# Optimization experiments

Measured on AMD Instinct MI355X. Metric: run time of the kernel, lower is better.

## Reference

```python
import jax, jax.numpy as jnp
import numpy as np

B, C, H, W = 64, 1024, 14, 14
DK, DV, NH = 512, 512, 8
NCLS = 32  # each class appears B//NCLS = 2 times -> no singleton labels


def setup_inputs() -> dict:
    key = jax.random.key(0)
    k1, k2, k3, k4 = jax.random.split(key, 4)
    dkh = DK // NH
    x = jax.random.normal(k1, (B, C, H, W), jnp.float32)
    W_qkv = jax.random.normal(k2, (2 * DK + DV, C), jnp.float32) * 0.02
    b_qkv = jnp.zeros((2 * DK + DV,), jnp.float32)
    key_rel_w = jax.random.normal(k3, (2 * W - 1, dkh), jnp.float32)
    key_rel_h = jax.random.normal(k4, (2 * H - 1, dkh), jnp.float32)
    # label-based pair index (training path of the torch module)
    rng = np.random.default_rng(0)
    labels = np.repeat(np.arange(NCLS), B // NCLS)
    rng.shuffle(labels)
    pair = np.empty(B, np.int32)
    for j in range(B):
        idx = np.nonzero(labels == labels[j])[0]
        pos = int(np.nonzero(idx == j)[0][0])
        pair[j] = idx[(pos + 1) % len(idx)]
    return {"x": x, "W_qkv": W_qkv, "b_qkv": b_qkv,
            "key_rel_w": key_rel_w, "key_rel_h": key_rel_h,
            "pair_index": jnp.asarray(pair)}


def rel_to_abs(x):
    b, nh, L, _ = x.shape
    x = jnp.pad(x, ((0, 0), (0, 0), (0, 0), (0, 1)))            # [b,nh,L,2L]
    flat = x.reshape(b, nh, L * 2 * L)
    flat = jnp.pad(flat, ((0, 0), (0, 0), (0, L - 1)))
    return flat.reshape(b, nh, L + 1, 2 * L - 1)[:, :, :L, L - 1:]


def relative_logits_1d(q, rel_k, Hd, Wd, nh, case):
    # q: [b, nh, Hd, Wd, dkh]; rel_k: [2*Wd-1, dkh]
    b = q.shape[0]
    rel = jnp.einsum('bhxyd,md->bhxym', q, rel_k)                 # [b,nh,Hd,Wd,2Wd-1]
    rel = rel_to_abs(rel.reshape(b, nh * Hd, Wd, 2 * Wd - 1))     # [b,nh*Hd,Wd,Wd]
    rel = rel.reshape(b, nh, Hd, Wd, Wd)[:, :, :, None]           # [b,nh,Hd,1,Wd,Wd]
    rel = jnp.broadcast_to(rel, (b, nh, Hd, Hd, Wd, Wd))
    if case == 'w':
        rel = jnp.swapaxes(rel, 3, 4)
    else:  # 'h'
        rel = jnp.swapaxes(rel, 2, 4)
        rel = jnp.swapaxes(rel, 4, 5)
        rel = jnp.swapaxes(rel, 3, 5)
    return rel.reshape(b, nh, Hd * Wd, Hd * Wd)


def reference(x, W_qkv, b_qkv, key_rel_w, key_rel_h, pair_index):
    b, c, h, w = x.shape
    nh, dk, dv = NH, DK, DV
    dkh = dk // nh
    # 1x1 conv == channel GEMM
    qkv = jnp.einsum('bchw,oc->bohw', x, W_qkv) + b_qkv[None, :, None, None]
    q = qkv[:, :dk].reshape(b, nh, dkh, h, w) * dkh ** (-0.5)
    k = qkv[:, dk:2 * dk].reshape(b, nh, dkh, h, w)
    flat_q = q.reshape(b, nh, dkh, h * w)
    flat_k = k.reshape(b, nh, dkh, h * w)
    flat_q = flat_q / jnp.linalg.norm(flat_q, axis=2, keepdims=True)
    flat_k = flat_k / jnp.linalg.norm(flat_k, axis=2, keepdims=True)
    q_avg = (flat_q[pair_index] + flat_q) * 0.5
    logits = jnp.einsum('bndq,bndk->bnqk', q_avg, flat_k)         # [b,nh,HW,HW]
    q_perm = jnp.transpose(q, (0, 1, 3, 4, 2))                    # [b,nh,h,w,dkh]
    w_rel = relative_logits_1d(q_perm, key_rel_w, h, w, nh, 'w')
    h_rel = relative_logits_1d(jnp.swapaxes(q_perm, 2, 3), key_rel_h, w, h, nh, 'h')
    logits = logits + h_rel + w_rel
    # combine_heads + mean over dim 1 == mean over (nh, query) axes
    mean_logits = jnp.mean(logits.reshape(b, nh, h * w, h, w), axis=(1, 2))  # [b,h,w]
    attn = jax.nn.softmax(mean_logits.reshape(b, -1), axis=-1).reshape(b, 1, h, w)
    return jnp.concatenate((x / 49.0, x * attn), axis=1)
```

## Files before the change

### kernel.cpp

```cpp
#include <hip/hip_runtime.h>
#include <hip/hip_bf16.h>
#include <math.h>

typedef unsigned short ushort_t;
using bf16x8 = __attribute__((ext_vector_type(8))) short;
using f32x4  = __attribute__((ext_vector_type(4))) float;

#define BATCH 64
#define CIN   1024
#define HH    14
#define WW    14
#define P     196
#define NHEAD 8
#define DKH   64
#define PPAD  224

#define OFF_Y16  0
#define N_Y16_F  6422528
#define OFF_XB   (OFF_Y16 + N_Y16_F)
#define N_XB_F   7340032
#define OFF_WB   (OFF_XB + N_XB_F)
#define N_WB_F   524288
#define OFF_INK  (OFF_WB + N_WB_F)
#define N_INK    (BATCH*NHEAD*P)
#define OFF_SQ   (OFF_INK + N_INK)
#define N_SQ     (BATCH*NHEAD*DKH)
#define OFF_QH   (OFF_SQ + N_SQ)
#define N_QH     (BATCH*HH*DKH)
#define OFF_QW   (OFF_QH + N_QH)
#define N_QW     (BATCH*WW*DKH)
#define OFF_AW   (OFF_QW + N_QW)
#define N_AW     (BATCH*WW)
#define OFF_AH   (OFF_AW + N_AW)
#define N_AH     (BATCH*HH)
#define OFF_ML   (OFF_AH + N_AH)
#define N_ML     (BATCH*P)
#define OFF_ATTN (OFF_ML + N_ML)
#define N_ATTN   (BATCH*P)
#define ZERO_FLOATS 129024

__device__ __forceinline__ ushort_t f2bf(float f) {
    union { float f; unsigned u; } v; v.f = f;
    unsigned r = v.u + 0x7fffu + ((v.u >> 16) & 1u);
    return (ushort_t)(r >> 16);
}
__device__ __forceinline__ float bf2f(ushort_t u) {
    union { unsigned u; float f; } v; v.u = ((unsigned)u) << 16; return v.f;
}
__device__ __forceinline__ void gll16(const ushort_t* g, ushort_t* l) {
    __builtin_amdgcn_global_load_lds(
        (const __attribute__((address_space(1))) void*)g,
        (__attribute__((address_space(3))) void*)l, 16, 0, 0);
}

__global__ __launch_bounds__(256) void k_convW(const float* __restrict__ Wq,
                                               ushort_t* __restrict__ Wb) {
    int i = blockIdx.x * 256 + threadIdx.x;
    const float4 v = ((const float4*)Wq)[i];
    ushort4 o;
    o.x = f2bf(v.x); o.y = f2bf(v.y); o.z = f2bf(v.z); o.w = f2bf(v.w);
    ((ushort4*)Wb)[i] = o;
}

__global__ __launch_bounds__(256) void k_trans(const float* __restrict__ x,
                                               ushort_t* __restrict__ Xb) {
    const int c0 = blockIdx.x * 64, p0 = blockIdx.y * 32, b = blockIdx.z;
    const int t = threadIdx.x;
    __shared__ float tile[64][33];
    const float* xb = x + (size_t)b * (CIN * P);
#pragma unroll
    for (int it = 0; it < 8; ++it) {
        int idx = t + it * 256;
        int c_l = idx >> 5, p_l = idx & 31;
        int p = p0 + p_l;
        tile[c_l][p_l] = (p < P) ? xb[(size_t)(c0 + c_l) * P + p] : 0.f;
    }
    __syncthreads();
    int c_chunk = (t & 7) * 8, p_l = t >> 3;
    ushort_t buf[8];
#pragma unroll
    for (int e = 0; e < 8; ++e) buf[e] = f2bf(tile[c_chunk + e][p_l]);
    *(uint4*)(Xb + ((size_t)b * PPAD + p0 + p_l) * CIN + c0 + c_chunk) = *(uint4*)buf;
}

__global__ __launch_bounds__(256, 4) void k_mfma(const ushort_t* __restrict__ Xb,
                                                 const ushort_t* __restrict__ Wb,
                                                 const float* __restrict__ bias,
                                                 ushort_t* __restrict__ Y16) {
    const int o0 = blockIdx.x * 128, r0 = blockIdx.y * 128;
    const int tid = threadIdx.x, w = tid >> 6, l = tid & 63;
    const int wm = w >> 1, wn = w & 1;
    __shared__ ushort_t xa[128 * 64];
    __shared__ ushort_t xw[128 * 64];
    f32x4 acc[4][4];
#pragma unroll
    for (int mf = 0; mf < 4; ++mf)
#pragma unroll
        for (int j = 0; j < 4; ++j) acc[mf][j] = (f32x4){0.f, 0.f, 0.f, 0.f};

    const ushort_t* Ab = Xb + (size_t)r0 * CIN;
    const ushort_t* Bb = Wb + (size_t)o0 * CIN;
    const int lrow = l >> 3, lch = (l & 7) * 8;

    for (int c0 = 0; c0 < CIN; c0 += 64) {
        if (c0) __syncthreads();
#pragma unroll
        for (int i = 0; i < 4; ++i) {
            int rowblk = (w * 4 + i) * 8;
            gll16(Ab + (size_t)(rowblk + lrow) * CIN + c0 + lch, xa + rowblk * 64);
        }
#pragma unroll
        for (int i = 0; i < 4; ++i) {
            int rowblk = (w * 4 + i) * 8;
            gll16(Bb + (size_t)(rowblk + lrow) * CIN + c0 + lch, xw + rowblk * 64);
        }
        __syncthreads();
#pragma unroll
        for (int kk = 0; kk < 2; ++kk) {
            bf16x8 bfrag[4];
#pragma unroll
            for (int j = 0; j < 4; ++j)
                bfrag[j] = *(const bf16x8*)(xw + (wn * 64 + j * 16 + (l & 15)) * 64 + kk * 32 + (l >> 4) * 8);
#pragma unroll
            for (int mf = 0; mf < 4; ++mf) {
                bf16x8 afrag = *(const bf16x8*)(xa + (wm * 64 + mf * 16 + (l & 15)) * 64 + kk * 32 + (l >> 4) * 8);
#pragma unroll
                for (int j = 0; j < 4; ++j)
                    acc[mf][j] = __builtin_amdgcn_mfma_f32_16x16x32_bf16(afrag, bfrag[j], acc[mf][j], 0, 0, 0);
            }
        }
    }
    const int oc = l & 15, pq = (l >> 4) * 4;
#pragma unroll
    for (int j = 0; j < 4; ++j) {
        int o = o0 + wn * 64 + j * 16 + oc;
        float bo = bias[o];
#pragma unroll
        for (int mf = 0; mf < 4; ++mf) {
            int r = r0 + wm * 64 + mf * 16 + pq;
            int b = r / PPAD;
            int p = r - b * PPAD;
            if (p < P) {
                ushort_t tmp[4];
#pragma unroll
                for (int e = 0; e < 4; ++e) tmp[e] = f2bf(acc[mf][j][e] + bo);
                *(ushort4*)(Y16 + ((size_t)b * 1024 + o) * P + p) = *(ushort4*)tmp;
            }
        }
    }
}

__global__ __launch_bounds__(256) void k_norm(const ushort_t* __restrict__ Y16,
                                              float* __restrict__ ink_g,
                                              float* __restrict__ sq_g,
                                              float* __restrict__ qh_g,
                                              float* __restrict__ qw_g) {
    const int bn = blockIdx.x, b = bn >> 3, n = bn & 7;
    const int tid = threadIdx.x;
    __shared__ ushort_t qs[64 * P];
    __shared__ float inq_s[P];
    __shared__ float part[4][64];
    const uint* Yq = (const uint*)(Y16 + ((size_t)b * 1024 + n * 64) * P);
    for (int i = tid; i < 64 * (P / 2); i += 256) ((uint*)qs)[i] = Yq[i];
    const ushort_t* Yk = Y16 + ((size_t)b * 1024 + 512 + n * 64) * P;
    const int p = tid, pc = (p < P) ? p : 0;
    float sk = 0.f;
    for (int d = 0; d < 64; ++d) { float v = bf2f(Yk[d * P + pc]); sk = fmaf(v, v, sk); }
    __syncthreads();
    float sq = 0.f;
    for (int d = 0; d < 64; ++d) { float v = bf2f(qs[d * P + pc]); sq = fmaf(v, v, sq); }
    if (p < P) { ink_g[bn * P + p] = rsqrtf(sk); inq_s[p] = rsqrtf(sq); }
    __syncthreads();
    {
        int d = tid & 63, q4 = tid >> 6;
        float s = 0.f;
        for (int i = 0; i < 49; ++i) {
            int pp = q4 * 49 + i;
            s = fmaf(bf2f(qs[d * P + pp]), inq_s[pp], s);
        }
        part[q4][d] = s;
    }
    __syncthreads();
    if (tid < 64) sq_g[bn * 64 + tid] = part[0][tid] + part[1][tid] + part[2][tid] + part[3][tid];
    for (int it = tid; it < 896; it += 256) {
        int d = it & 63, xx = it >> 6;
        float s = 0.f;
#pragma unroll
        for (int y = 0; y < WW; ++y) s += bf2f(qs[d * P + xx * WW + y]);
        atomicAdd(&qh_g[(b * HH + xx) * 64 + d], s * 0.125f);
    }
    for (int it = tid; it < 896; it += 256) {
        int d = it & 63, y = it >> 6;
        float s = 0.f;
#pragma unroll
        for (int xx = 0; xx < HH; ++xx) s += bf2f(qs[d * P + xx * WW + y]);
        atomicAdd(&qw_g[(b * WW + y) * 64 + d], s * 0.125f);
    }
}

__global__ __launch_bounds__(512) void k_rel(const float* __restrict__ qh_g,
                                             const float* __restrict__ qw_g,
                                             const float* __restrict__ relw,
                                             const float* __restrict__ relh,
                                             float* __restrict__ Aw_g,
                                             float* __restrict__ Ah_g) {
    const int b = blockIdx.x, t = threadIdx.x;
    if (t < 196) {
        int X = t / 14, y = t % 14;
        const float* qw = qw_g + (b * WW + y) * 64;
        const float* rw = relw + (13 + X - y) * 64;
        float s = 0.f;
#pragma unroll 8
        for (int d = 0; d < 64; ++d) s = fmaf(qw[d], rw[d], s);
        atomicAdd(&Aw_g[b * WW + X], s);
    } else if (t >= 256 && t < 452) {
        int i = t - 256, X = i / 14, xr = i % 14;
        const float* qh = qh_g + (b * HH + xr) * 64;
        const float* rh = relh + (13 + X - xr) * 64;
        float s = 0.f;
#pragma unroll 8
        for (int d = 0; d < 64; ++d) s = fmaf(qh[d], rh[d], s);
        atomicAdd(&Ah_g[b * HH + X], s);
    }
}

__global__ __launch_bounds__(256) void k_dot(const ushort_t* __restrict__ Y16,
                                             const float* __restrict__ ink_g,
                                             const float* __restrict__ sq_g,
                                             const int*   __restrict__ pair,
                                             float* __restrict__ ml) {
    const int bn = blockIdx.x, b = bn >> 3, n = bn & 7;
    const int tid = threadIdx.x;
    __shared__ float Sav[64];
    if (tid < 64) {
        int pb = pair[b];
        Sav[tid] = 0.5f * (sq_g[bn * 64 + tid] + sq_g[(pb * 8 + n) * 64 + tid]);
    }
    __syncthreads();
    const int p = tid;
    if (p < P) {
        const ushort_t* Yk = Y16 + ((size_t)b * 1024 + 512 + n * 64) * P;
        float s = 0.f;
#pragma unroll 8
        for (int d = 0; d < 64; ++d) s = fmaf(Sav[d], bf2f(Yk[d * P + p]), s);
        atomicAdd(&ml[b * P + p], s * ink_g[bn * P + p]);
    }
}

__global__ __launch_bounds__(256) void k_soft(const float* __restrict__ ml,
                                              const float* __restrict__ Aw_g,
                                              const float* __restrict__ Ah_g,
                                              float* __restrict__ attn_g) {
    const int b = blockIdx.x, tid = threadIdx.x;
    __shared__ float red[256];
    const int p = tid;
    float v = -1e30f;
    if (p < P) v = (ml[b * P + p] + Ah_g[b * HH + p / WW] + Aw_g[b * WW + p % WW]) * (1.f / 1568.f);
    red[tid] = v; __syncthreads();
    for (int s = 128; s > 0; s >>= 1) { if (tid < s) red[tid] = fmaxf(red[tid], red[tid + s]); __syncthreads(); }
    float mx = red[0]; __syncthreads();
    float e = (p < P) ? expf(v - mx) : 0.f;
    red[tid] = e; __syncthreads();
    for (int s = 128; s > 0; s >>= 1) { if (tid < s) red[tid] += red[tid + s]; __syncthreads(); }
    if (p < P) attn_g[b * P + p] = e / red[0];
}

__global__ __launch_bounds__(256) void k_out(const float* __restrict__ x,
                                             const float* __restrict__ attn_g,
                                             float* __restrict__ out) {
    const int total4 = BATCH * CIN * P / 4;
    const int stride = gridDim.x * 256;
    const float4* x4 = (const float4*)x;
    const float4* a4 = (const float4*)attn_g;
    float4* o4 = (float4*)out;
    for (int i4 = blockIdx.x * 256 + threadIdx.x; i4 < total4; i4 += stride) {
        int i = i4 * 4;
        int b = i / (CIN * P);
        int r = i - b * (CIN * P);
        int p0 = r % P;
        float4 xv = x4[i4];
        float4 at = a4[(b * P + p0) >> 2];
        float4 o1 = make_float4(xv.x * (1.f/49.f), xv.y * (1.f/49.f),
                                xv.z * (1.f/49.f), xv.w * (1.f/49.f));
        float4 o2 = make_float4(xv.x * at.x, xv.y * at.y, xv.z * at.z, xv.w * at.w);
        o4[(b * (2 * CIN * P) + r) >> 2] = o1;
        o4[(b * (2 * CIN * P) + CIN * P + r) >> 2] = o2;
    }
}

extern "C" void kernel_launch(void* const* d_in, const int* in_sizes, int n_in,
                              void* d_out, int out_size, void* d_ws, size_t ws_size,
                              hipStream_t stream) {
    const float* x    = (const float*)d_in[0];
    const float* Wq   = (const float*)d_in[1];
    const float* bias = (const float*)d_in[2];
    const float* relw = (const float*)d_in[3];
    const float* relh = (const float*)d_in[4];
    const int*   pair = (const int*)d_in[5];
    float* out = (float*)d_out;
    float* ws  = (float*)d_ws;

    ushort_t* Y16 = (ushort_t*)(ws + OFF_Y16);
    ushort_t* Xb  = (ushort_t*)(ws + OFF_XB);
    ushort_t* Wb  = (ushort_t*)(ws + OFF_WB);
    float* ink  = ws + OFF_INK;
    float* sq   = ws + OFF_SQ;
    float* qh   = ws + OFF_QH;
    float* qw   = ws + OFF_QW;
    float* Aw   = ws + OFF_AW;
    float* Ah   = ws + OFF_AH;
    float* ml   = ws + OFF_ML;
    float* attn = ws + OFF_ATTN;

    hipMemsetAsync(ws + OFF_QH, 0, ZERO_FLOATS * sizeof(float), stream);
    k_convW<<<1024, 256, 0, stream>>>(Wq, Wb);
    k_trans<<<dim3(16, 7, 64), 256, 0, stream>>>(x, Xb);
    k_mfma <<<dim3(8, 112), 256, 0, stream>>>(Xb, Wb, bias, Y16);
    k_norm <<<BATCH * NHEAD, 256, 0, stream>>>(Y16, ink, sq, qh, qw);
    k_rel  <<<BATCH, 512, 0, stream>>>(qh, qw, relw, relh, Aw, Ah);
    k_dot  <<<BATCH * NHEAD, 256, 0, stream>>>(Y16, ink, sq, pair, ml);
    k_soft <<<BATCH, 256, 0, stream>>>(ml, Aw, Ah, attn);
    k_out  <<<2048, 256, 0, stream>>>(x, attn, out);
}
```

Measured before the change: 129.4 us.

## Replace global atomics with per-head partials and fuse rel-logits into softmax kernel

k_norm and k_dot now write per-(batch,head) partial sums to separate workspace slots instead of atomically accumulating into shared per-batch buffers. A new k_attn2 kernel reduces the 8 head partials, computes the relative-position terms in shared memory, and does the softmax, replacing k_rel and k_soft. This removes the memset, one kernel launch and global atomic contention. In exchange the partial buffers are larger and the final per-batch kernel does more serial reduction work.

```diff
diff --git a/kernel.cpp b/kernel.cpp
--- a/kernel.cpp
+++ b/kernel.cpp
@@ -25,19 +25,14 @@
 #define N_INK    (BATCH*NHEAD*P)
 #define OFF_SQ   (OFF_INK + N_INK)
 #define N_SQ     (BATCH*NHEAD*DKH)
-#define OFF_QH   (OFF_SQ + N_SQ)
-#define N_QH     (BATCH*HH*DKH)
-#define OFF_QW   (OFF_QH + N_QH)
-#define N_QW     (BATCH*WW*DKH)
-#define OFF_AW   (OFF_QW + N_QW)
-#define N_AW     (BATCH*WW)
-#define OFF_AH   (OFF_AW + N_AW)
-#define N_AH     (BATCH*HH)
-#define OFF_ML   (OFF_AH + N_AH)
-#define N_ML     (BATCH*P)
-#define OFF_ATTN (OFF_ML + N_ML)
+#define OFF_QHP  (OFF_SQ + N_SQ)
+#define N_QHP    (BATCH*NHEAD*HH*DKH)
+#define OFF_QWP  (OFF_QHP + N_QHP)
+#define N_QWP    (BATCH*NHEAD*WW*DKH)
+#define OFF_DOTP (OFF_QWP + N_QWP)
+#define N_DOTP   (BATCH*NHEAD*P)
+#define OFF_ATTN (OFF_DOTP + N_DOTP)
 #define N_ATTN   (BATCH*P)
-#define ZERO_FLOATS 129024
 
 __device__ __forceinline__ ushort_t f2bf(float f) {
     union { float f; unsigned u; } v; v.f = f;
@@ -153,8 +148,8 @@
 __global__ __launch_bounds__(256) void k_norm(const ushort_t* __restrict__ Y16,
                                               float* __restrict__ ink_g,
                                               float* __restrict__ sq_g,
-                                              float* __restrict__ qh_g,
-                                              float* __restrict__ qw_g) {
+                                              float* __restrict__ qhp,
+                                              float* __restrict__ qwp) {
     const int bn = blockIdx.x, b = bn >> 3, n = bn & 7;
     const int tid = threadIdx.x;
     __shared__ ushort_t qs[64 * P];
@@ -187,40 +182,14 @@
         float s = 0.f;
 #pragma unroll
         for (int y = 0; y < WW; ++y) s += bf2f(qs[d * P + xx * WW + y]);
-        atomicAdd(&qh_g[(b * HH + xx) * 64 + d], s * 0.125f);
+        qhp[bn * 896 + it] = s * 0.125f;
     }
     for (int it = tid; it < 896; it += 256) {
         int d = it & 63, y = it >> 6;
         float s = 0.f;
 #pragma unroll
         for (int xx = 0; xx < HH; ++xx) s += bf2f(qs[d * P + xx * WW + y]);
-        atomicAdd(&qw_g[(b * WW + y) * 64 + d], s * 0.125f);
-    }
-}
-
-__global__ __launch_bounds__(512) void k_rel(const float* __restrict__ qh_g,
-                                             const float* __restrict__ qw_g,
-                                             const float* __restrict__ relw,
-                                             const float* __restrict__ relh,
-                                             float* __restrict__ Aw_g,
-                                             float* __restrict__ Ah_g) {
-    const int b = blockIdx.x, t = threadIdx.x;
-    if (t < 196) {
-        int X = t / 14, y = t % 14;
-        const float* qw = qw_g + (b * WW + y) * 64;
-        const float* rw = relw + (13 + X - y) * 64;
-        float s = 0.f;
-#pragma unroll 8
-        for (int d = 0; d < 64; ++d) s = fmaf(qw[d], rw[d], s);
-        atomicAdd(&Aw_g[b * WW + X], s);
-    } else if (t >= 256 && t < 452) {
-        int i = t - 256, X = i / 14, xr = i % 14;
-        const float* qh = qh_g + (b * HH + xr) * 64;
-        const float* rh = relh + (13 + X - xr) * 64;
-        float s = 0.f;
-#pragma unroll 8
-        for (int d = 0; d < 64; ++d) s = fmaf(qh[d], rh[d], s);
-        atomicAdd(&Ah_g[b * HH + X], s);
+        qwp[bn * 896 + it] = s * 0.125f;
     }
 }
 
@@ -228,7 +197,7 @@
                                              const float* __restrict__ ink_g,
                                              const float* __restrict__ sq_g,
                                              const int*   __restrict__ pair,
-                                             float* __restrict__ ml) {
+                                             float* __restrict__ dotp) {
     const int bn = blockIdx.x, b = bn >> 3, n = bn & 7;
     const int tid = threadIdx.x;
     __shared__ float Sav[64];
@@ -243,19 +212,55 @@
         float s = 0.f;
 #pragma unroll 8
         for (int d = 0; d < 64; ++d) s = fmaf(Sav[d], bf2f(Yk[d * P + p]), s);
-        atomicAdd(&ml[b * P + p], s * ink_g[bn * P + p]);
-    }
-}
-
-__global__ __launch_bounds__(256) void k_soft(const float* __restrict__ ml,
-                                              const float* __restrict__ Aw_g,
-                                              const float* __restrict__ Ah_g,
-                                              float* __restrict__ attn_g) {
+        dotp[bn * P + p] = s * ink_g[bn * P + p];
+    }
+}
+
+__global__ __launch_bounds__(256) void k_attn2(const float* __restrict__ dotp,
+                                               const float* __restrict__ qhp,
+                                               const float* __restrict__ qwp,
+                                               const float* __restrict__ relw,
+                                               const float* __restrict__ relh,
+                                               float* __restrict__ attn_g) {
     const int b = blockIdx.x, tid = threadIdx.x;
+    __shared__ float qhs[896], qws[896];
+    __shared__ float Aw[WW], Ah[HH];
     __shared__ float red[256];
+    for (int i = tid; i < 896; i += 256) {
+        float sh = 0.f, sw = 0.f;
+#pragma unroll
+        for (int n = 0; n < 8; ++n) {
+            sh += qhp[(size_t)(b * 8 + n) * 896 + i];
+            sw += qwp[(size_t)(b * 8 + n) * 896 + i];
+        }
+        qhs[i] = sh; qws[i] = sw;
+    }
+    if (tid < WW) { Aw[tid] = 0.f; Ah[tid] = 0.f; }
+    __syncthreads();
+    if (tid < 196) {
+        int X = tid / 14, y = tid % 14;
+        const float* qp = &qws[y * 64];
+        const float* rw = relw + (13 + X - y) * 64;
+        float s = 0.f;
+#pragma unroll 8
+        for (int d = 0; d < 64; ++d) s = fmaf(qp[d], rw[d], s);
+        atomicAdd(&Aw[X], s);
+        const float* hp = &qhs[y * 64];
+        const float* rh = relh + (13 + X - y) * 64;
+        float s2 = 0.f;
+#pragma unroll 8
+        for (int d = 0; d < 64; ++d) s2 = fmaf(hp[d], rh[d], s2);
+        atomicAdd(&Ah[X], s2);
+    }
+    __syncthreads();
     const int p = tid;
     float v = -1e30f;
-    if (p < P) v = (ml[b * P + p] + Ah_g[b * HH + p / WW] + Aw_g[b * WW + p % WW]) * (1.f / 1568.f);
+    if (p < P) {
+        float dot = 0.f;
+#pragma unroll
+        for (int n = 0; n < 8; ++n) dot += dotp[(size_t)(b * 8 + n) * P + p];
+        v = (dot + Ah[p / WW] + Aw[p % WW]) * (1.f / 1568.f);
+    }
     red[tid] = v; __syncthreads();
     for (int s = 128; s > 0; s >>= 1) { if (tid < s) red[tid] = fmaxf(red[tid], red[tid + s]); __syncthreads(); }
     float mx = red[0]; __syncthreads();
@@ -305,20 +310,16 @@
     ushort_t* Wb  = (ushort_t*)(ws + OFF_WB);
     float* ink  = ws + OFF_INK;
     float* sq   = ws + OFF_SQ;
-    float* qh   = ws + OFF_QH;
-    float* qw   = ws + OFF_QW;
-    float* Aw   = ws + OFF_AW;
-    float* Ah   = ws + OFF_AH;
-    float* ml   = ws + OFF_ML;
+    float* qhp  = ws + OFF_QHP;
+    float* qwp  = ws + OFF_QWP;
+    float* dotp = ws + OFF_DOTP;
     float* attn = ws + OFF_ATTN;
 
-    hipMemsetAsync(ws + OFF_QH, 0, ZERO_FLOATS * sizeof(float), stream);
     k_convW<<<1024, 256, 0, stream>>>(Wq, Wb);
     k_trans<<<dim3(16, 7, 64), 256, 0, stream>>>(x, Xb);
     k_mfma <<<dim3(8, 112), 256, 0, stream>>>(Xb, Wb, bias, Y16);
-    k_norm <<<BATCH * NHEAD, 256, 0, stream>>>(Y16, ink, sq, qh, qw);
-    k_rel  <<<BATCH, 512, 0, stream>>>(qh, qw, relw, relh, Aw, Ah);
-    k_dot  <<<BATCH * NHEAD, 256, 0, stream>>>(Y16, ink, sq, pair, ml);
-    k_soft <<<BATCH, 256, 0, stream>>>(ml, Aw, Ah, attn);
+    k_norm <<<BATCH * NHEAD, 256, 0, stream>>>(Y16, ink, sq, qhp, qwp);
+    k_dot  <<<BATCH * NHEAD, 256, 0, stream>>>(Y16, ink, sq, pair, dotp);
+    k_attn2<<<BATCH, 256, 0, stream>>>(dotp, qhp, qwp, relw, relh, attn);
     k_out  <<<2048, 256, 0, stream>>>(x, attn, out);
 }
```

Result: faster. 118.6 us (-8.3%).
